# Kernel optimization log

Measured on AMD Instinct MI355X. Metric: run time of the kernel, lower is better.

## Reference

```python
import jax, jax.numpy as jnp
import numpy as np

B, L, F = 16, 1024, 64
D = 256          # d_model (expand_factor=1 -> d_inner == d_model)
S = 2            # num_scales
N = 16           # state_size
H = 32           # fc hidden
EPS = 1e-5


def setup_inputs() -> dict:
    key = jax.random.key(0)
    ks = jax.random.split(key, 20)
    g = lambda i, shape, s=0.05: jax.random.normal(ks[i], shape, dtype=jnp.float32) * s
    return {
        "x": jax.random.normal(ks[0], (B, L, F), dtype=jnp.float32),
        "W_in": g(1, (F, D)), "b_in": jnp.zeros((D,), jnp.float32),
        # per-scale liquid-Mamba params, stacked over scales
        "Wd": g(2, (S, D, D)), "bd": jnp.zeros((S, D), jnp.float32),
        "WB": g(3, (S, D, N)), "WC": g(4, (S, D, N)),
        "Wtau": g(5, (S, D, D)),
        "A_log": jnp.broadcast_to(jnp.log(jnp.arange(1, N + 1, dtype=jnp.float32)), (S, D, N)).copy(),
        "Dp": jnp.ones((S, D), jnp.float32),
        "Wout": g(6, (S, D, D)),
        # head
        "ln_g": jnp.ones((D,), jnp.float32), "ln_b": jnp.zeros((D,), jnp.float32),
        "W1": g(7, (D, H)), "b1": jnp.zeros((H,), jnp.float32),
        "W2": g(8, (H, 1)), "b2": jnp.zeros((1,), jnp.float32),
    }


def _liquid_ssm(x, Wd, bd, WB, WC, Wtau, A_log, Dp, Wout):
    # x: [B,L,D] -> y: [B,L,D]. Selective scan with liquid time-constant gate.
    delta = jax.nn.softplus(jnp.einsum('bld,de->ble', x, Wd) + bd)   # [B,L,D]
    tau = jax.nn.sigmoid(jnp.einsum('bld,de->ble', x, Wtau))          # liquid gate
    delta = delta * tau
    Bm = jnp.einsum('bld,dn->bln', x, WB)                             # [B,L,N]
    Cm = jnp.einsum('bld,dn->bln', x, WC)                             # [B,L,N]
    A = -jnp.exp(A_log)                                               # [D,N]
    dA = jnp.exp(delta[..., None] * A)                                # [B,L,D,N]
    dBx = delta[..., None] * Bm[:, :, None, :] * x[..., None]         # [B,L,D,N]

    def step(h, inp):
        a_t, bx_t, c_t = inp                                          # [B,D,N],[B,D,N],[B,N]
        h = a_t * h + bx_t
        y = jnp.einsum('bdn,bn->bd', h, c_t)
        return h, y

    h0 = jnp.zeros((x.shape[0], x.shape[2], A.shape[1]), x.dtype)
    _, ys = jax.lax.scan(step, h0,
                         (dA.transpose(1, 0, 2, 3), dBx.transpose(1, 0, 2, 3), Cm.transpose(1, 0, 2)))
    y = ys.transpose(1, 0, 2) + x * Dp                                # skip connection
    return jnp.einsum('bld,de->ble', y, Wout)


def reference(x, W_in, b_in, Wd, bd, WB, WC, Wtau, A_log, Dp, Wout,
              ln_g, ln_b, W1, b1, W2, b2):
    h = jnp.einsum('blf,fd->bld', x, W_in) + b_in                     # input projection
    outs = [_liquid_ssm(h, Wd[s], bd[s], WB[s], WC[s], Wtau[s], A_log[s], Dp[s], Wout[s])
            for s in range(Wd.shape[0])]
    mamba_out = sum(outs) / len(outs)                                 # average over scales
    last = mamba_out[:, -1, :]                                        # [B,D]
    mu = jnp.mean(last, axis=-1, keepdims=True)
    var = jnp.var(last, axis=-1, keepdims=True)
    z = (last - mu) * jax.lax.rsqrt(var + EPS) * ln_g + ln_b          # LayerNorm
    z = jax.nn.relu(z @ W1 + b1)                                      # dropout is identity in eval
    return z @ W2 + b2                                                # [B,1]
```

## Files before the change

kernel.cpp:

```cpp
#include <hip/hip_runtime.h>
#include <hip/hip_bf16.h>
#include <math.h>

#define B_   16
#define L_   1024
#define F_   64
#define D_   256
#define S_   2
#define N_   16
#define H_   32
#define EPS_ 1e-5f
#define BL_  (B_*L_)
#define NCH_ 16
#define TC_  (L_/NCH_)
#define TSTR_ 68
#define LOG2E_ 1.44269504088896340736f
#define XBLK_ (BL_*F_/1024)

typedef __attribute__((ext_vector_type(8))) short  bf16x8;
typedef __attribute__((ext_vector_type(4))) float  f32x4;
typedef __attribute__((ext_vector_type(2))) float  f32x2;

typedef const __attribute__((address_space(1))) void* gas_ptr;
typedef __attribute__((address_space(3))) void*       las_ptr;

#if defined(__has_builtin)
# if __has_builtin(__builtin_amdgcn_exp2f)
#  define EXP2(x) __builtin_amdgcn_exp2f(x)
#  define ASCALE_ LOG2E_
# endif
#endif
#ifndef EXP2
# define EXP2(x) __expf(x)
# define ASCALE_ 1.0f
#endif

__device__ inline void async_copy16(const void* g, void* l) {
    __builtin_amdgcn_global_load_lds((gas_ptr)g, (las_ptr)l, 16, 0, 0);
}

__device__ inline unsigned short f2bf_rne(float x) {
    union { float f; unsigned u; } v; v.f = x;
    unsigned r = v.u + 0x7fff + ((v.u >> 16) & 1);
    return (unsigned short)(r >> 16);
}

__global__ __launch_bounds__(256) void k_prep(const float* __restrict__ x,
                                              const float* __restrict__ Win,
                                              const float* __restrict__ bin,
                                              const float* __restrict__ Wd,
                                              const float* __restrict__ bd,
                                              const float* __restrict__ Wt,
                                              const float* __restrict__ WB,
                                              unsigned short* __restrict__ x_hi,
                                              unsigned short* __restrict__ Weff_hi,
                                              float* __restrict__ bias_eff,
                                              unsigned short* __restrict__ WinT_hi,
                                              unsigned short* __restrict__ WBe_hi,
                                              float* __restrict__ bbias)
{
    const int blk = blockIdx.x;
    const int tid = threadIdx.x;

    if (blk < XBLK_) {
        const int i = (blk * 256 + tid) * 4;
        float4 v = *(const float4*)(x + i);
        ushort4 h4;
        h4.x = f2bf_rne(v.x);
        h4.y = f2bf_rne(v.y);
        h4.z = f2bf_rne(v.z);
        h4.w = f2bf_rne(v.w);
        *(ushort4*)(x_hi + i) = h4;
        return;
    }

    const int job4 = blk - XBLK_;
    const int j    = tid >> 6;
    const int f    = tid & 63;
    const int job  = job4 * 4 + j;

    __shared__ float col[4][D_];

    if (job < 1024) {
        const int s = job >> 9, n = job & 511;
        const float* W = (n < 256) ? (Wd + (size_t)s * D_ * D_) : (Wt + (size_t)s * D_ * D_);
        const int e = n & 255;
        for (int d = f; d < D_; d += 64) col[j][d] = W[(size_t)d * D_ + e];
        __syncthreads();
        float a = 0.f;
        for (int d = 0; d < D_; ++d) a += Win[(size_t)f * D_ + d] * col[j][d];
        Weff_hi[((size_t)s * 512 + n) * F_ + f] = f2bf_rne(a);
        if (f == 0) {
            float bb = 0.f;
            for (int d = 0; d < D_; ++d) bb += bin[d] * col[j][d];
            if (n < 256) bb += bd[s * D_ + e];
            bias_eff[s * 512 + n] = bb;
        }
    } else if (job < 1024 + D_) {
        const int d = job - 1024;
        WinT_hi[(size_t)d * F_ + f] = f2bf_rne(Win[(size_t)f * D_ + d]);
    } else {
        const int idx = job - (1024 + D_);
        const int s = idx >> 4, n = idx & 15;
        const float* wb = WB + (size_t)s * D_ * N_;
        float a = 0.f;
        for (int d = 0; d < D_; ++d) a += Win[(size_t)f * D_ + d] * wb[(size_t)d * N_ + n];
        WBe_hi[((size_t)s * N_ + n) * F_ + f] = f2bf_rne(a);
        if (f == 0) {
            float bb = 0.f;
            for (int d = 0; d < D_; ++d) bb += bin[d] * wb[(size_t)d * N_ + n];
            bbias[s * N_ + n] = bb;
        }
    }
}

__global__ __launch_bounds__(256) void k_fused_scan(
        const unsigned short* __restrict__ x_hi,
        const unsigned short* __restrict__ Weff_hi,
        const unsigned short* __restrict__ WinT_hi,
        const unsigned short* __restrict__ WBe_hi,
        const float* __restrict__ bias_eff,
        const float* __restrict__ bin,
        const float* __restrict__ bbias,
        const float* __restrict__ A_log,
        float* __restrict__ part,
        float* __restrict__ csum)
{
    const int dtile = blockIdx.x >> 4;
    const int c     = blockIdx.x & 15;
    const int b     = blockIdx.y;
    const int s     = blockIdx.z;
    const int d0    = dtile * 16;
    const int tid   = threadIdx.x;
    const int wid   = tid >> 6;
    const int lane  = tid & 63;
    const int l15   = lane & 15;
    const int quad  = lane >> 4;
    const int dl    = tid & 15;
    const int nl    = tid >> 4;

    __shared__ unsigned short Wh[64 * F_];
    __shared__ float sdl[16][TSTR_];
    __shared__ float sq [16][TSTR_];
    __shared__ float sb [16][TSTR_];

    const int r8 = lane >> 3;
    const int c8 = lane & 7;

    #pragma unroll
    for (int call = 0; call < 2; ++call) {
        const int rr = call * 8 + r8;
        const int ar = wid * 16 + rr;
        const int lc = (c8 - ar) & 7;
        const unsigned short* gh;
        if (wid == 0)      gh = Weff_hi + ((size_t)s * 512 + d0 + rr) * F_ + lc * 8;
        else if (wid == 1) gh = Weff_hi + ((size_t)s * 512 + 256 + d0 + rr) * F_ + lc * 8;
        else if (wid == 2) gh = WinT_hi + ((size_t)(d0 + rr)) * F_ + lc * 8;
        else               gh = WBe_hi + ((size_t)s * N_ + rr) * F_ + lc * 8;
        async_copy16(gh, &Wh[(wid * 16 + call * 8) * F_]);
    }

    const float bias_d = bias_eff[s * 512 + d0 + l15];
    const float bias_t = bias_eff[s * 512 + 256 + d0 + l15];
    const float bin_v  = bin[d0 + l15];
    const float bb_v   = bbias[s * N_ + l15];
    const float A2 = -__expf(A_log[((size_t)s * D_ + d0 + dl) * N_ + nl]) * ASCALE_;

    const int qoff = quad * 8;
    bf16x8 fah0, fah1;
    {
        const size_t rowb = ((size_t)b * L_ + c * TC_ + wid * 16 + l15) * F_;
        fah0 = *(const bf16x8*)(x_hi + rowb + qoff);
        fah1 = *(const bf16x8*)(x_hi + rowb + 32 + qoff);
    }
    __syncthreads();

    f32x4 acc[4];
    #pragma unroll
    for (int g = 0; g < 4; ++g) acc[g] = (f32x4){0.f, 0.f, 0.f, 0.f};
    #pragma unroll
    for (int ks = 0; ks < 2; ++ks) {
        bf16x8 ah = ks ? fah1 : fah0;
        #pragma unroll
        for (int g = 0; g < 4; ++g) {
            const int brow = g * 16 + l15;
            const int pcB  = ((ks * 4 + quad) + brow) & 7;
            bf16x8 bh = *(const bf16x8*)&Wh[brow * F_ + pcB * 8];
            acc[g] = __builtin_amdgcn_mfma_f32_16x16x32_bf16(ah, bh, acc[g], 0, 0, 0);
        }
    }

    {
        f32x4 wd_, wq_, wb_;
        #pragma unroll
        for (int r = 0; r < 4; ++r) {
            const float pd  = acc[0][r] + bias_d;
            const float sp  = fmaxf(pd, 0.f) + __logf(1.f + __expf(-fabsf(pd)));
            const float sg  = 1.f / (1.f + __expf(-(acc[1][r] + bias_t)));
            const float dlt = sp * sg;
            const float hv  = acc[2][r] + bin_v;
            wd_[r] = dlt;
            wq_[r] = dlt * hv;
            wb_[r] = acc[3][r] + bb_v;
        }
        const int tcol = wid * 16 + quad * 4;
        *(f32x4*)&sdl[l15][tcol] = wd_;
        *(f32x4*)&sq [l15][tcol] = wq_;
        *(f32x4*)&sb [l15][tcol] = wb_;
    }
    __syncthreads();

    f32x2 stA0 = {0.f, 0.f}, stA1 = {0.f, 0.f};
    f32x2 stB0 = {0.f, 0.f}, stB1 = {0.f, 0.f};
    float As0 = 0.f, As1 = 0.f;
    #pragma unroll
    for (int it = 7; it >= 0; --it) {
        {
            const int tt = it * 4;
            f32x4 dp = *(const f32x4*)&sdl[dl][tt];
            f32x4 qp = *(const f32x4*)&sq [dl][tt];
            f32x4 bp = *(const f32x4*)&sb [nl][tt];
            const float a2v = fmaf(A2, dp.w, As0);
            const float a1v = fmaf(A2, dp.z, a2v);
            const float a0v = fmaf(A2, dp.y, a1v);
            f32x2 e01, e23;
            e23.y = EXP2(As0);
            e23.x = EXP2(a2v);
            e01.y = EXP2(a1v);
            e01.x = EXP2(a0v);
            f32x2 q01 = {qp.x, qp.y}, q23 = {qp.z, qp.w};
            f32x2 b01 = {bp.x, bp.y}, b23 = {bp.z, bp.w};
            stA0 = q01 * b01 * e01 + stA0;
            stA1 = q23 * b23 * e23 + stA1;
            As0 = fmaf(A2, dp.x, a0v);
        }
        {
            const int tt = 32 + it * 4;
            f32x4 dp = *(const f32x4*)&sdl[dl][tt];
            f32x4 qp = *(const f32x4*)&sq [dl][tt];
            f32x4 bp = *(const f32x4*)&sb [nl][tt];
            const float a2v = fmaf(A2, dp.w, As1);
            const float a1v = fmaf(A2, dp.z, a2v);
            const float a0v = fmaf(A2, dp.y, a1v);
            f32x2 e01, e23;
            e23.y = EXP2(As1);
            e23.x = EXP2(a2v);
            e01.y = EXP2(a1v);
            e01.x = EXP2(a0v);
            f32x2 q01 = {qp.x, qp.y}, q23 = {qp.z, qp.w};
            f32x2 b01 = {bp.x, bp.y}, b23 = {bp.z, bp.w};
            stB0 = q01 * b01 * e01 + stB0;
            stB1 = q23 * b23 * e23 + stB1;
            As1 = fmaf(A2, dp.x, a0v);
        }
    }
    const float seg0 = stA0.x + stA0.y + stA1.x + stA1.y;
    const float seg1 = stB0.x + stB0.y + stB1.x + stB1.y;
    const float state = seg1 + EXP2(As1) * seg0;
    const float Atot  = As1 + As0;

    const size_t pb = ((size_t)s * B_ + b) * NCH_ + c;
    part[(pb * D_ + d0 + dl) * N_ + nl] = state;
    if (nl == 0)
        csum[pb * D_ + d0 + dl] = Atot / A2;
}

__global__ __launch_bounds__(256) void k_ys(const float* __restrict__ x,
                                            const float* __restrict__ Win,
                                            const float* __restrict__ bin,
                                            const float* __restrict__ part,
                                            const float* __restrict__ csum,
                                            const float* __restrict__ A_log,
                                            const float* __restrict__ WC,
                                            const float* __restrict__ Dp,
                                            float* __restrict__ ys)
{
    const int s   = blockIdx.x;
    const int b   = blockIdx.y;
    const int d0  = blockIdx.z * 16;
    const int tid = threadIdx.x;
    const int dl  = tid & 15;
    const int nl  = tid >> 4;
    const int d   = d0 + dl;

    __shared__ float xr[F_];
    __shared__ float hl[D_];
    __shared__ float cred[N_][17];
    __shared__ float cm[N_];
    __shared__ float csh[NCH_][16];
    __shared__ float red[N_][17];

    if (tid < F_) xr[tid] = x[((size_t)b * L_ + (L_ - 1)) * F_ + tid];
    __syncthreads();

    {
        float a = bin[tid];
        for (int f = 0; f < F_; ++f) a += xr[f] * Win[(size_t)f * D_ + tid];
        hl[tid] = a;
    }
    __syncthreads();

    {
        const int n  = tid & 15;
        const int dq = tid >> 4;
        float a = 0.f;
        for (int dd = dq * 16; dd < dq * 16 + 16; ++dd)
            a += hl[dd] * WC[((size_t)s * D_ + dd) * N_ + n];
        cred[n][dq] = a;
        const size_t cbase0 = ((size_t)s * B_ + b) * NCH_;
        csh[tid >> 4][tid & 15] = csum[(cbase0 + (tid >> 4)) * D_ + d0 + (tid & 15)];
    }
    __syncthreads();
    if (tid < N_) {
        float a = 0.f;
        #pragma unroll
        for (int q = 0; q < 16; ++q) a += cred[tid][q];
        cm[tid] = a;
    }
    __syncthreads();

    const float A = -__expf(A_log[((size_t)s * D_ + d) * N_ + nl]);
    const size_t cbase = ((size_t)s * B_ + b) * NCH_;
    float acc = 0.f;
    float tail = 0.f;
    #pragma unroll
    for (int c = NCH_ - 1; c >= 0; --c) {
        const float p = part[((cbase + c) * D_ + d) * N_ + nl];
        acc += __expf(A * tail) * p;
        tail += csh[c][dl];
    }
    red[nl][dl] = cm[nl] * acc;
    __syncthreads();

    if (tid < 16) {
        float a = 0.f;
        #pragma unroll
        for (int n = 0; n < N_; ++n) a += red[n][tid];
        const int dd = d0 + tid;
        ys[((size_t)s * B_ + b) * D_ + dd] = a + hl[dd] * Dp[s * D_ + dd];
    }
}

__global__ __launch_bounds__(256) void k_last(const float* __restrict__ ys,
                                              const float* __restrict__ Wout,
                                              float* __restrict__ last)
{
    const int b  = blockIdx.x;
    const int e0 = blockIdx.y * 64;
    const int tid = threadIdx.x;
    const int e  = tid & 63;
    const int kq = tid >> 6;

    __shared__ float ysl[S_ * D_];
    __shared__ float red[4][64];

    #pragma unroll
    for (int j = tid; j < S_ * D_; j += 256) {
        const int ss = j >> 8, dd = j & 255;
        ysl[j] = ys[((size_t)ss * B_ + b) * D_ + dd];
    }
    __syncthreads();

    float a = 0.f;
    for (int k = kq * 128; k < kq * 128 + 128; ++k) {
        const int ss = k >> 8, dd = k & 255;
        a += ysl[k] * Wout[((size_t)ss * D_ + dd) * D_ + e0 + e];
    }
    red[kq][e] = a;
    __syncthreads();
    if (kq == 0) {
        const float v = (red[0][e] + red[1][e] + red[2][e] + red[3][e]) * (1.f / S_);
        last[(size_t)b * D_ + e0 + e] = v;
    }
}

__global__ __launch_bounds__(256) void k_head(const float* __restrict__ last,
                                              const float* __restrict__ ln_g,
                                              const float* __restrict__ ln_b,
                                              const float* __restrict__ W1,
                                              const float* __restrict__ b1,
                                              const float* __restrict__ W2,
                                              const float* __restrict__ b2,
                                              float* __restrict__ out)
{
    const int b   = blockIdx.x;
    const int tid = threadIdx.x;

    __shared__ float zv[D_];
    __shared__ float red1[256];
    __shared__ float red2[256];
    __shared__ float r1[H_];

    const float v = last[(size_t)b * D_ + tid];
    red1[tid] = v;
    red2[tid] = v * v;
    __syncthreads();
    for (int off = 128; off > 0; off >>= 1) {
        if (tid < off) { red1[tid] += red1[tid + off]; red2[tid] += red2[tid + off]; }
        __syncthreads();
    }
    const float mu  = red1[0] * (1.f / D_);
    const float var = red2[0] * (1.f / D_) - mu * mu;
    const float z = (v - mu) * rsqrtf(var + EPS_) * ln_g[tid] + ln_b[tid];
    zv[tid] = z;
    __syncthreads();

    if (tid < H_) {
        float a = b1[tid];
        for (int e = 0; e < D_; ++e) a += zv[e] * W1[(size_t)e * H_ + tid];
        r1[tid] = fmaxf(a, 0.f);
    }
    __syncthreads();
    if (tid == 0) {
        float a = b2[0];
        for (int j = 0; j < H_; ++j) a += r1[j] * W2[j];
        out[b] = a;
    }
}

extern "C" void kernel_launch(void* const* d_in, const int* in_sizes, int n_in,
                              void* d_out, int out_size, void* d_ws, size_t ws_size,
                              hipStream_t stream)
{
    const float* x     = (const float*)d_in[0];
    const float* Win   = (const float*)d_in[1];
    const float* bin   = (const float*)d_in[2];
    const float* Wd    = (const float*)d_in[3];
    const float* bd    = (const float*)d_in[4];
    const float* WB    = (const float*)d_in[5];
    const float* WC    = (const float*)d_in[6];
    const float* Wtau  = (const float*)d_in[7];
    const float* A_log = (const float*)d_in[8];
    const float* Dp    = (const float*)d_in[9];
    const float* Wout  = (const float*)d_in[10];
    const float* ln_g  = (const float*)d_in[11];
    const float* ln_b  = (const float*)d_in[12];
    const float* W1    = (const float*)d_in[13];
    const float* b1    = (const float*)d_in[14];
    const float* W2    = (const float*)d_in[15];
    const float* b2    = (const float*)d_in[16];
    float* out = (float*)d_out;

    char* ws = (char*)d_ws;
    const size_t MB = 1024 * 1024;
    const size_t KB = 1024;
    unsigned short* x_hi     = (unsigned short*)(ws);
    unsigned short* Weff_hi  = (unsigned short*)(ws + 2 * MB);
    unsigned short* WinT_hi  = (unsigned short*)(ws + 2 * MB + 128 * KB);
    unsigned short* WBe_hi   = (unsigned short*)(ws + 2 * MB + 160 * KB);
    float*          bias_eff = (float*)(ws + 2 * MB + 164 * KB);
    float*          bbias    = (float*)(ws + 2 * MB + 168 * KB);
    float*          part     = (float*)(ws + 3 * MB);
    float*          csum     = (float*)(ws + 11 * MB);
    float*          ysbuf    = (float*)(ws + 11 * MB + 512 * KB);
    float*          lastbuf  = (float*)(ws + 11 * MB + 544 * KB);

    hipLaunchKernelGGL(k_prep, dim3(XBLK_ + 328), dim3(256), 0, stream,
                       x, Win, bin, Wd, bd, Wtau, WB,
                       x_hi, Weff_hi, bias_eff, WinT_hi, WBe_hi, bbias);
    hipLaunchKernelGGL(k_fused_scan, dim3((D_ / 16) * NCH_, B_, S_), dim3(256), 0, stream,
                       x_hi, Weff_hi, WinT_hi, WBe_hi,
                       bias_eff, bin, bbias, A_log, part, csum);
    hipLaunchKernelGGL(k_ys,   dim3(S_, B_, D_ / 16), dim3(256), 0, stream,
                       x, Win, bin, part, csum, A_log, WC, Dp, ysbuf);
    hipLaunchKernelGGL(k_last, dim3(B_, 4), dim3(256), 0, stream, ysbuf, Wout, lastbuf);
    hipLaunchKernelGGL(k_head, dim3(B_), dim3(256), 0, stream,
                       lastbuf, ln_g, ln_b, W1, b1, W2, b2, out);
}
```

Baseline: 163.2 us.

## Fuse ys, last and head kernels into one per-batch tail kernel

Replaces the three small post-scan kernels (k_ys, k_last, k_head) with a single k_tail kernel that runs one block per batch. It combines the chunk partial states, applies the skip term, projects through Wout, and runs LayerNorm plus the MLP head. Intermediate results stay in shared memory instead of global buffers. This removes two launches and their global round trips, at the cost of far less parallelism: 16 blocks each walk all 256 channels with per-thread loops over chunks and state. The W1 product is also split across all threads with a shared-memory reduction.

```diff
diff --git a/kernel.cpp b/kernel.cpp
--- a/kernel.cpp
+++ b/kernel.cpp
@@ -265,116 +265,15 @@
         csum[pb * D_ + d0 + dl] = Atot / A2;
 }
 
-__global__ __launch_bounds__(256) void k_ys(const float* __restrict__ x,
-                                            const float* __restrict__ Win,
-                                            const float* __restrict__ bin,
-                                            const float* __restrict__ part,
-                                            const float* __restrict__ csum,
-                                            const float* __restrict__ A_log,
-                                            const float* __restrict__ WC,
-                                            const float* __restrict__ Dp,
-                                            float* __restrict__ ys)
-{
-    const int s   = blockIdx.x;
-    const int b   = blockIdx.y;
-    const int d0  = blockIdx.z * 16;
-    const int tid = threadIdx.x;
-    const int dl  = tid & 15;
-    const int nl  = tid >> 4;
-    const int d   = d0 + dl;
-
-    __shared__ float xr[F_];
-    __shared__ float hl[D_];
-    __shared__ float cred[N_][17];
-    __shared__ float cm[N_];
-    __shared__ float csh[NCH_][16];
-    __shared__ float red[N_][17];
-
-    if (tid < F_) xr[tid] = x[((size_t)b * L_ + (L_ - 1)) * F_ + tid];
-    __syncthreads();
-
-    {
-        float a = bin[tid];
-        for (int f = 0; f < F_; ++f) a += xr[f] * Win[(size_t)f * D_ + tid];
-        hl[tid] = a;
-    }
-    __syncthreads();
-
-    {
-        const int n  = tid & 15;
-        const int dq = tid >> 4;
-        float a = 0.f;
-        for (int dd = dq * 16; dd < dq * 16 + 16; ++dd)
-            a += hl[dd] * WC[((size_t)s * D_ + dd) * N_ + n];
-        cred[n][dq] = a;
-        const size_t cbase0 = ((size_t)s * B_ + b) * NCH_;
-        csh[tid >> 4][tid & 15] = csum[(cbase0 + (tid >> 4)) * D_ + d0 + (tid & 15)];
-    }
-    __syncthreads();
-    if (tid < N_) {
-        float a = 0.f;
-        #pragma unroll
-        for (int q = 0; q < 16; ++q) a += cred[tid][q];
-        cm[tid] = a;
-    }
-    __syncthreads();
-
-    const float A = -__expf(A_log[((size_t)s * D_ + d) * N_ + nl]);
-    const size_t cbase = ((size_t)s * B_ + b) * NCH_;
-    float acc = 0.f;
-    float tail = 0.f;
-    #pragma unroll
-    for (int c = NCH_ - 1; c >= 0; --c) {
-        const float p = part[((cbase + c) * D_ + d) * N_ + nl];
-        acc += __expf(A * tail) * p;
-        tail += csh[c][dl];
-    }
-    red[nl][dl] = cm[nl] * acc;
-    __syncthreads();
-
-    if (tid < 16) {
-        float a = 0.f;
-        #pragma unroll
-        for (int n = 0; n < N_; ++n) a += red[n][tid];
-        const int dd = d0 + tid;
-        ys[((size_t)s * B_ + b) * D_ + dd] = a + hl[dd] * Dp[s * D_ + dd];
-    }
-}
-
-__global__ __launch_bounds__(256) void k_last(const float* __restrict__ ys,
+__global__ __launch_bounds__(256) void k_tail(const float* __restrict__ x,
+                                              const float* __restrict__ Win,
+                                              const float* __restrict__ bin,
+                                              const float* __restrict__ part,
+                                              const float* __restrict__ csum,
+                                              const float* __restrict__ A_log,
+                                              const float* __restrict__ WC,
+                                              const float* __restrict__ Dp,
                                               const float* __restrict__ Wout,
-                                              float* __restrict__ last)
-{
-    const int b  = blockIdx.x;
-    const int e0 = blockIdx.y * 64;
-    const int tid = threadIdx.x;
-    const int e  = tid & 63;
-    const int kq = tid >> 6;
-
-    __shared__ float ysl[S_ * D_];
-    __shared__ float red[4][64];
-
-    #pragma unroll
-    for (int j = tid; j < S_ * D_; j += 256) {
-        const int ss = j >> 8, dd = j & 255;
-        ysl[j] = ys[((size_t)ss * B_ + b) * D_ + dd];
-    }
-    __syncthreads();
-
-    float a = 0.f;
-    for (int k = kq * 128; k < kq * 128 + 128; ++k) {
-        const int ss = k >> 8, dd = k & 255;
-        a += ysl[k] * Wout[((size_t)ss * D_ + dd) * D_ + e0 + e];
-    }
-    red[kq][e] = a;
-    __syncthreads();
-    if (kq == 0) {
-        const float v = (red[0][e] + red[1][e] + red[2][e] + red[3][e]) * (1.f / S_);
-        last[(size_t)b * D_ + e0 + e] = v;
-    }
-}
-
-__global__ __launch_bounds__(256) void k_head(const float* __restrict__ last,
                                               const float* __restrict__ ln_g,
                                               const float* __restrict__ ln_b,
                                               const float* __restrict__ W1,
@@ -386,12 +285,100 @@
     const int b   = blockIdx.x;
     const int tid = threadIdx.x;
 
+    __shared__ float xr[F_];
+    __shared__ float hl[D_];
+    __shared__ float csh[S_][NCH_][D_];
+    __shared__ float credS[S_][N_][16];
+    __shared__ float cm[S_][N_];
+    __shared__ float ysl[S_][D_];
     __shared__ float zv[D_];
     __shared__ float red1[256];
     __shared__ float red2[256];
+    __shared__ float mred[8][33];
     __shared__ float r1[H_];
 
-    const float v = last[(size_t)b * D_ + tid];
+    if (tid < F_) xr[tid] = x[((size_t)b * L_ + (L_ - 1)) * F_ + tid];
+    for (int j = tid * 4; j < S_ * NCH_ * D_; j += 256 * 4) {
+        const int s  = j >> 12;
+        const int c  = (j >> 8) & 15;
+        const int dd = j & 255;
+        *(f32x4*)&csh[s][c][dd] =
+            *(const f32x4*)&csum[(((size_t)s * B_ + b) * NCH_ + c) * D_ + dd];
+    }
+    __syncthreads();
+
+    {
+        float a = bin[tid];
+        for (int f = 0; f < F_; ++f) a += xr[f] * Win[(size_t)f * D_ + tid];
+        hl[tid] = a;
+    }
+    __syncthreads();
+
+    {
+        const int n  = tid & 15;
+        const int dq = tid >> 4;
+        float a0 = 0.f, a1 = 0.f;
+        for (int dd = dq * 16; dd < dq * 16 + 16; ++dd) {
+            const float h = hl[dd];
+            a0 += h * WC[((size_t)0 * D_ + dd) * N_ + n];
+            a1 += h * WC[((size_t)1 * D_ + dd) * N_ + n];
+        }
+        credS[0][n][dq] = a0;
+        credS[1][n][dq] = a1;
+    }
+    __syncthreads();
+    if (tid < S_ * N_) {
+        const int s = tid >> 4, n = tid & 15;
+        float a = 0.f;
+        #pragma unroll
+        for (int q = 0; q < 16; ++q) a += credS[s][n][q];
+        cm[s][n] = a;
+    }
+    __syncthreads();
+
+    {
+        const int d = tid;
+        float A2a[N_], A2b[N_], cma[N_], cmb[N_];
+        #pragma unroll
+        for (int n = 0; n < N_; ++n) {
+            A2a[n] = -__expf(A_log[((size_t)0 * D_ + d) * N_ + n]) * ASCALE_;
+            A2b[n] = -__expf(A_log[((size_t)1 * D_ + d) * N_ + n]) * ASCALE_;
+            cma[n] = cm[0][n];
+            cmb[n] = cm[1][n];
+        }
+        float y0 = 0.f, y1 = 0.f;
+        float t0 = 0.f, t1 = 0.f;
+        for (int c = NCH_ - 1; c >= 0; --c) {
+            const float* p0 = part + (((size_t)(0 * B_ + b) * NCH_ + c) * D_ + d) * N_;
+            const float* p1 = part + (((size_t)(1 * B_ + b) * NCH_ + c) * D_ + d) * N_;
+            #pragma unroll
+            for (int nq = 0; nq < 4; ++nq) {
+                f32x4 pa = *(const f32x4*)(p0 + nq * 4);
+                f32x4 pb = *(const f32x4*)(p1 + nq * 4);
+                #pragma unroll
+                for (int r = 0; r < 4; ++r) {
+                    const int n = nq * 4 + r;
+                    y0 = fmaf(cma[n] * pa[r], EXP2(A2a[n] * t0), y0);
+                    y1 = fmaf(cmb[n] * pb[r], EXP2(A2b[n] * t1), y1);
+                }
+            }
+            t0 += csh[0][c][d];
+            t1 += csh[1][c][d];
+        }
+        ysl[0][d] = y0 + hl[d] * Dp[0 * D_ + d];
+        ysl[1][d] = y1 + hl[d] * Dp[1 * D_ + d];
+    }
+    __syncthreads();
+
+    float v;
+    {
+        const float* yf = &ysl[0][0];
+        float a = 0.f;
+        for (int k = 0; k < S_ * D_; ++k)
+            a += yf[k] * Wout[(size_t)k * D_ + tid];
+        v = a * (1.f / S_);
+    }
+
     red1[tid] = v;
     red2[tid] = v * v;
     __syncthreads();
@@ -405,9 +392,21 @@
     zv[tid] = z;
     __syncthreads();
 
+    {
+        const int hh = tid & 31, q = tid >> 5;
+        float a = 0.f;
+        #pragma unroll
+        for (int e0 = 0; e0 < 32; ++e0) {
+            const int e = q * 32 + e0;
+            a += zv[e] * W1[(size_t)e * H_ + hh];
+        }
+        mred[q][hh] = a;
+    }
+    __syncthreads();
     if (tid < H_) {
         float a = b1[tid];
-        for (int e = 0; e < D_; ++e) a += zv[e] * W1[(size_t)e * H_ + tid];
+        #pragma unroll
+        for (int q = 0; q < 8; ++q) a += mred[q][tid];
         r1[tid] = fmaxf(a, 0.f);
     }
     __syncthreads();
@@ -452,8 +451,6 @@
     float*          bbias    = (float*)(ws + 2 * MB + 168 * KB);
     float*          part     = (float*)(ws + 3 * MB);
     float*          csum     = (float*)(ws + 11 * MB);
-    float*          ysbuf    = (float*)(ws + 11 * MB + 512 * KB);
-    float*          lastbuf  = (float*)(ws + 11 * MB + 544 * KB);
 
     hipLaunchKernelGGL(k_prep, dim3(XBLK_ + 328), dim3(256), 0, stream,
                        x, Win, bin, Wd, bd, Wtau, WB,
@@ -461,9 +458,7 @@
     hipLaunchKernelGGL(k_fused_scan, dim3((D_ / 16) * NCH_, B_, S_), dim3(256), 0, stream,
                        x_hi, Weff_hi, WinT_hi, WBe_hi,
                        bias_eff, bin, bbias, A_log, part, csum);
-    hipLaunchKernelGGL(k_ys,   dim3(S_, B_, D_ / 16), dim3(256), 0, stream,
-                       x, Win, bin, part, csum, A_log, WC, Dp, ysbuf);
-    hipLaunchKernelGGL(k_last, dim3(B_, 4), dim3(256), 0, stream, ysbuf, Wout, lastbuf);
-    hipLaunchKernelGGL(k_head, dim3(B_), dim3(256), 0, stream,
-                       lastbuf, ln_g, ln_b, W1, b1, W2, b2, out);
-}
+    hipLaunchKernelGGL(k_tail, dim3(B_), dim3(256), 0, stream,
+                       x, Win, bin, part, csum, A_log, WC, Dp, Wout,
+                       ln_g, ln_b, W1, b1, W2, b2, out);
+}
```

Result: slower. 173.4 us (+6.2%).
